# Performance work log

Measured on AMD Instinct MI355X. Metric: run time of the kernel, lower is better.

Reference implementation:

```python
import jax, jax.numpy as jnp
import numpy as np

ALPHA = 20.0 / 100.0  # dt / tau
ONE_MINUS_ALPHA = 1.0 - ALPHA
GAIN = 1.0


def setup_inputs() -> dict:
    key = jax.random.key(0)
    ks = jax.random.split(key, 6)
    seq_len, batch, input_size, hidden_size = 512, 64, 512, 1024
    s_in = 1.0 / np.sqrt(input_size)
    s_hh = 1.0 / np.sqrt(hidden_size)
    return {
        "x": jax.random.normal(ks[0], (seq_len, batch, input_size), jnp.float32),
        "hidden": jnp.zeros((batch, hidden_size), jnp.float32),
        "W_in": jax.random.normal(ks[1], (hidden_size, input_size), jnp.float32) * s_in,
        "b_in": jax.random.normal(ks[2], (hidden_size,), jnp.float32) * s_in,
        "W_hh": jax.random.normal(ks[3], (hidden_size, hidden_size), jnp.float32) * s_hh,
        "b_hh": jax.random.normal(ks[4], (hidden_size,), jnp.float32) * s_hh,
    }


def reference(x, hidden, W_in, b_in, W_hh, b_hh):
    # Precompute input projections for all timesteps in one big GEMM:
    # (T, B, I) @ (I, H) -> (T, B, H)
    x_proj = jnp.einsum("tbi,hi->tbh", x, W_in) + b_in

    def step(h, xp_t):
        pre = h @ W_hh.T + b_hh + xp_t  # (B, H)
        h_new = h * ONE_MINUS_ALPHA + ALPHA * jax.nn.sigmoid(GAIN * pre)
        return h_new, h_new

    h_last, output = jax.lax.scan(step, hidden, x_proj)
    return output, h_last
```

## Files before the change

kernel.cpp:

```cpp
#include <hip/hip_runtime.h>
#include <hip/hip_bf16.h>


typedef __attribute__((ext_vector_type(8))) short short8;
typedef __attribute__((ext_vector_type(4))) float f32x4;
typedef unsigned long long ull;

#define TT 512
#define BB 64
#define II 512
#define HH 1024

__device__ __forceinline__ short f2bf(float f) {
  unsigned u = __builtin_bit_cast(unsigned, f);
  u += 0x7fffu + ((u >> 16) & 1u);
  return (short)(u >> 16);
}

__device__ __forceinline__ short8 pack8(const float* p) {
  short8 s;
  s[0] = f2bf(p[0]); s[1] = f2bf(p[1]); s[2] = f2bf(p[2]); s[3] = f2bf(p[3]);
  s[4] = f2bf(p[4]); s[5] = f2bf(p[5]); s[6] = f2bf(p[6]); s[7] = f2bf(p[7]);
  return s;
}

__global__ __launch_bounds__(256, 1) void rnn_persist(
    const float* __restrict__ x, const float* __restrict__ h0,
    const float* __restrict__ Win, const float* __restrict__ bin,
    const float* __restrict__ Whh, const float* __restrict__ bhh,
    float* __restrict__ out, short* __restrict__ ring0,
    short* __restrict__ ring1, int* __restrict__ flags) {
  __shared__ short Wl[64 * 1024];
  __shared__ float Pr[4 * 16 * 68];

  const int bid = blockIdx.x;
  const int r = bid & 3, g = bid >> 2;
  const int tid = threadIdx.x;
  const int l = tid & 63, w = tid >> 6;
  const int lr = l & 15, lg = l >> 4;
  const int n0 = g * 64;

  for (int j = 0; j < 32; ++j) {
    int c = j * 256 + tid;
    int kc = c & 127, n = c >> 7;
    const float* src = Whh + (size_t)(n0 + n) * HH + kc * 8;
    float4 v0 = *(const float4*)src;
    float4 v1 = *(const float4*)(src + 4);
    short* d = Wl + (((size_t)kc * 64 + n) << 3);
    d[0] = f2bf(v0.x); d[1] = f2bf(v0.y); d[2] = f2bf(v0.z); d[3] = f2bf(v0.w);
    d[4] = f2bf(v1.x); d[5] = f2bf(v1.y); d[6] = f2bf(v1.z); d[7] = f2bf(v1.w);
  }

  short8 wf[4][4];
  #pragma unroll
  for (int nt = 0; nt < 4; ++nt) {
    #pragma unroll
    for (int kc = 0; kc < 4; ++kc) {
      const float* src = Win + (size_t)(n0 + nt * 16 + lr) * II + w * 128 + kc * 32 + lg * 8;
      float tmp[8];
      *(float4*)&tmp[0] = *(const float4*)src;
      *(float4*)&tmp[4] = *(const float4*)(src + 4);
      wf[nt][kc] = pack8(tmp);
    }
  }

  const int brow = tid >> 4;
  const int c0 = (tid & 15) * 4;
  const size_t oidx = (size_t)(16 * r + brow) * HH + n0 + c0;
  const size_t ringoff =
      (((size_t)(r * 128 + 8 * g + (c0 >> 3)) * 16 + brow) << 3) + (c0 & 7);

  f32x4 bias;
  #pragma unroll
  for (int k = 0; k < 4; ++k)
    bias[k] = bin[n0 + c0 + k] + bhh[n0 + c0 + k];

  f32x4 hpv;
  {
    float4 v = *(const float4*)(h0 + oidx);
    hpv[0] = v.x; hpv[1] = v.y; hpv[2] = v.z; hpv[3] = v.w;
    ull u = (ull)(unsigned short)f2bf(v.x)
          | ((ull)(unsigned short)f2bf(v.y) << 16)
          | ((ull)(unsigned short)f2bf(v.z) << 32)
          | ((ull)(unsigned short)f2bf(v.w) << 48);
    __hip_atomic_store((ull*)(ring0 + ringoff), u,
                       __ATOMIC_RELAXED, __HIP_MEMORY_SCOPE_AGENT);
  }

  float xs[4][8];
  {
    const float* xb = x + ((size_t)(16 * r + lr)) * II + w * 128 + lg * 8;
    #pragma unroll
    for (int kc = 0; kc < 4; ++kc) {
      *(float4*)&xs[kc][0] = *(const float4*)(xb + kc * 32);
      *(float4*)&xs[kc][4] = *(const float4*)(xb + kc * 32 + 4);
    }
  }

  __syncthreads();
  if (tid == 0)
    __hip_atomic_store(&flags[bid], 1, __ATOMIC_RELAXED, __HIP_MEMORY_SCOPE_AGENT);

  const int fidx = 16 * w + 4 * (l & 3) + r;
  const short* bW = Wl + ((((size_t)(32 * w + lg)) * 64 + lr) << 3);
  const size_t abase = ((((size_t)(r * 128 + 32 * w + lg)) * 16 + lr) << 3);

  for (int t = 0; t < TT; ++t) {
    short* rc = (t & 1) ? ring1 : ring0;
    short* rn = (t & 1) ? ring0 : ring1;
    float* outt = out + (size_t)t * (BB * HH);

    f32x4 acc[4];
    acc[0] = acc[1] = acc[2] = acc[3] = (f32x4){0.f, 0.f, 0.f, 0.f};
    #pragma unroll
    for (int kc = 0; kc < 4; ++kc) {
      short8 xa = pack8(xs[kc]);
      acc[0] = __builtin_amdgcn_mfma_f32_16x16x32_bf16(xa, wf[0][kc], acc[0], 0, 0, 0);
      acc[1] = __builtin_amdgcn_mfma_f32_16x16x32_bf16(xa, wf[1][kc], acc[1], 0, 0, 0);
      acc[2] = __builtin_amdgcn_mfma_f32_16x16x32_bf16(xa, wf[2][kc], acc[2], 0, 0, 0);
      acc[3] = __builtin_amdgcn_mfma_f32_16x16x32_bf16(xa, wf[3][kc], acc[3], 0, 0, 0);
    }

    {
      int target = t + 1;
      while (!__all(__hip_atomic_load(&flags[fidx], __ATOMIC_RELAXED,
                                      __HIP_MEMORY_SCOPE_AGENT) >= target))
        __builtin_amdgcn_s_sleep(1);
    }

    const short* ar = rc + abase;
    const short* ar2 = ar + 2048;
    int4 fa[8];
#define LDA(I, BASE, OFF) \
    asm volatile("global_load_dwordx4 %0, %1, off offset:%2 sc0 sc1" \
                 : "=v"(fa[I]) : "v"(BASE), "n"(OFF))
    LDA(0, ar, 0); LDA(1, ar, 1024); LDA(2, ar, 2048); LDA(3, ar, 3072);
    LDA(4, ar2, 0); LDA(5, ar2, 1024); LDA(6, ar2, 2048); LDA(7, ar2, 3072);
#undef LDA
    asm volatile("s_waitcnt vmcnt(0)" ::: "memory");
    __builtin_amdgcn_sched_barrier(0);

    #pragma unroll
    for (int i = 0; i < 8; ++i) {
      short8 a = __builtin_bit_cast(short8, fa[i]);
      acc[0] = __builtin_amdgcn_mfma_f32_16x16x32_bf16(
          a, *(const short8*)(bW + i * 2048 + 0),   acc[0], 0, 0, 0);
      acc[1] = __builtin_amdgcn_mfma_f32_16x16x32_bf16(
          a, *(const short8*)(bW + i * 2048 + 128), acc[1], 0, 0, 0);
      acc[2] = __builtin_amdgcn_mfma_f32_16x16x32_bf16(
          a, *(const short8*)(bW + i * 2048 + 256), acc[2], 0, 0, 0);
      acc[3] = __builtin_amdgcn_mfma_f32_16x16x32_bf16(
          a, *(const short8*)(bW + i * 2048 + 384), acc[3], 0, 0, 0);
    }

    float* pw = Pr + w * 1088;
    #pragma unroll
    for (int nt = 0; nt < 4; ++nt) {
      #pragma unroll
      for (int jj = 0; jj < 4; ++jj)
        pw[(lg * 4 + jj) * 68 + nt * 16 + lr] = acc[nt][jj];
    }
    __syncthreads();

    const float* pb = Pr + brow * 68 + c0;
    f32x4 s = *(const f32x4*)(pb)
            + *(const f32x4*)(pb + 1088)
            + *(const f32x4*)(pb + 2176)
            + *(const f32x4*)(pb + 3264);
    f32x4 hn;
    #pragma unroll
    for (int k = 0; k < 4; ++k) {
      float pre = s[k] + bias[k];
      float sg = 1.f / (1.f + __expf(-pre));
      hn[k] = 0.8f * hpv[k] + 0.2f * sg;
    }

    {
      ull u = (ull)(unsigned short)f2bf(hn[0])
            | ((ull)(unsigned short)f2bf(hn[1]) << 16)
            | ((ull)(unsigned short)f2bf(hn[2]) << 32)
            | ((ull)(unsigned short)f2bf(hn[3]) << 48);
      __hip_atomic_store((ull*)(rn + ringoff), u,
                         __ATOMIC_RELAXED, __HIP_MEMORY_SCOPE_AGENT);
    }
    asm volatile("s_waitcnt vmcnt(0)" ::: "memory");
    __syncthreads();
    if (tid == 0)
      __hip_atomic_store(&flags[bid], t + 2, __ATOMIC_RELAXED, __HIP_MEMORY_SCOPE_AGENT);

    *(float4*)(outt + oidx) = *(float4*)&hn;
    if (t == TT - 1) {
      *(float4*)(out + (size_t)TT * BB * HH + oidx) = *(float4*)&hn;
    } else {
      const float* xb = x + ((size_t)(t + 1) * BB + 16 * r + lr) * II + w * 128 + lg * 8;
      #pragma unroll
      for (int kc = 0; kc < 4; ++kc) {
        *(float4*)&xs[kc][0] = *(const float4*)(xb + kc * 32);
        *(float4*)&xs[kc][4] = *(const float4*)(xb + kc * 32 + 4);
      }
    }
    hpv = hn;
  }
}

extern "C" void kernel_launch(void* const* d_in, const int* in_sizes, int n_in,
                              void* d_out, int out_size, void* d_ws, size_t ws_size,
                              hipStream_t stream) {
  const float* x   = (const float*)d_in[0];
  const float* h0  = (const float*)d_in[1];
  const float* Win = (const float*)d_in[2];
  const float* bin = (const float*)d_in[3];
  const float* Whh = (const float*)d_in[4];
  const float* bhh = (const float*)d_in[5];
  float* out = (float*)d_out;

  int* flags = (int*)d_ws;
  short* ring0 = (short*)((char*)d_ws + 256);
  short* ring1 = ring0 + BB * HH;

  hipMemsetAsync(d_ws, 0, 256, stream);
  rnn_persist<<<dim3(64), 256, 0, stream>>>(x, h0, Win, bin, Whh, bhh,
                                            out, ring0, ring1, flags);
}
```

Before: 1.873 ms.

## Add producer warps computing input projection two steps ahead into shared ring

Doubles the block to 512 threads and splits it into 256 consumer threads, which run the recurrent matmul and update, and 256 producer threads. The producers compute the input projection x_t·W_in^T for step t+2 into a 3-slot shared-memory buffer. This takes the input-projection MFMAs and the x loads off the consumer's critical path between flag waits. In exchange there are more threads per CU and extra shared memory, and all 512 threads must reach the two __syncthreads per step, so the producers' work has to fit inside the consumers' step time.

```diff
diff --git a/kernel.cpp b/kernel.cpp
--- a/kernel.cpp
+++ b/kernel.cpp
@@ -24,7 +24,7 @@
   return s;
 }
 
-__global__ __launch_bounds__(256, 1) void rnn_persist(
+__global__ __launch_bounds__(512, 1) void rnn_persist(
     const float* __restrict__ x, const float* __restrict__ h0,
     const float* __restrict__ Win, const float* __restrict__ bin,
     const float* __restrict__ Whh, const float* __restrict__ bhh,
@@ -32,68 +32,82 @@
     short* __restrict__ ring1, int* __restrict__ flags) {
   __shared__ short Wl[64 * 1024];
   __shared__ float Pr[4 * 16 * 68];
+  __shared__ float Xp[3][16 * 68];
 
   const int bid = blockIdx.x;
   const int r = bid & 3, g = bid >> 2;
   const int tid = threadIdx.x;
-  const int l = tid & 63, w = tid >> 6;
+  const bool cons = (tid < 256);
+  const int l = tid & 63;
   const int lr = l & 15, lg = l >> 4;
   const int n0 = g * 64;
 
-  for (int j = 0; j < 32; ++j) {
-    int c = j * 256 + tid;
-    int kc = c & 127, n = c >> 7;
-    const float* src = Whh + (size_t)(n0 + n) * HH + kc * 8;
-    float4 v0 = *(const float4*)src;
-    float4 v1 = *(const float4*)(src + 4);
-    short* d = Wl + (((size_t)kc * 64 + n) << 3);
-    d[0] = f2bf(v0.x); d[1] = f2bf(v0.y); d[2] = f2bf(v0.z); d[3] = f2bf(v0.w);
-    d[4] = f2bf(v1.x); d[5] = f2bf(v1.y); d[6] = f2bf(v1.z); d[7] = f2bf(v1.w);
-  }
-
-  short8 wf[4][4];
-  #pragma unroll
-  for (int nt = 0; nt < 4; ++nt) {
+  f32x4 hpv, bias;
+  size_t oidx = 0, ringoff = 0;
+  int fidx = 0;
+  const short* bW = nullptr;
+  size_t abase = 0;
+  int brow = 0, c0 = 0;
+
+  short8 wf[16];
+  int pw = 0;
+
+  if (cons) {
+    const int w = tid >> 6;
+    for (int j = 0; j < 32; ++j) {
+      int c = j * 256 + tid;
+      int kc = c & 127, n = c >> 7;
+      const float* src = Whh + (size_t)(n0 + n) * HH + kc * 8;
+      float4 v0 = *(const float4*)src;
+      float4 v1 = *(const float4*)(src + 4);
+      short* d = Wl + (((size_t)kc * 64 + n) << 3);
+      d[0] = f2bf(v0.x); d[1] = f2bf(v0.y); d[2] = f2bf(v0.z); d[3] = f2bf(v0.w);
+      d[4] = f2bf(v1.x); d[5] = f2bf(v1.y); d[6] = f2bf(v1.z); d[7] = f2bf(v1.w);
+    }
+    brow = tid >> 4;
+    c0 = (tid & 15) * 4;
+    oidx = (size_t)(16 * r + brow) * HH + n0 + c0;
+    ringoff = (((size_t)(r * 128 + 8 * g + (c0 >> 3)) * 16 + brow) << 3) + (c0 & 7);
     #pragma unroll
-    for (int kc = 0; kc < 4; ++kc) {
-      const float* src = Win + (size_t)(n0 + nt * 16 + lr) * II + w * 128 + kc * 32 + lg * 8;
+    for (int k = 0; k < 4; ++k)
+      bias[k] = bin[n0 + c0 + k] + bhh[n0 + c0 + k];
+    {
+      float4 v = *(const float4*)(h0 + oidx);
+      hpv[0] = v.x; hpv[1] = v.y; hpv[2] = v.z; hpv[3] = v.w;
+      ull u = (ull)(unsigned short)f2bf(v.x)
+            | ((ull)(unsigned short)f2bf(v.y) << 16)
+            | ((ull)(unsigned short)f2bf(v.z) << 32)
+            | ((ull)(unsigned short)f2bf(v.w) << 48);
+      __hip_atomic_store((ull*)(ring0 + ringoff), u,
+                         __ATOMIC_RELAXED, __HIP_MEMORY_SCOPE_AGENT);
+    }
+    fidx = 16 * w + 4 * (l & 3) + r;
+    bW = Wl + ((((size_t)(32 * w + lg)) * 64 + lr) << 3);
+    abase = ((((size_t)(r * 128 + 32 * w + lg)) * 16 + lr) << 3);
+  } else {
+    pw = (tid >> 6) & 3;
+    #pragma unroll
+    for (int kidx = 0; kidx < 16; ++kidx) {
+      const float* src = Win + (size_t)(n0 + 16 * pw + lr) * II + kidx * 32 + lg * 8;
       float tmp[8];
       *(float4*)&tmp[0] = *(const float4*)src;
       *(float4*)&tmp[4] = *(const float4*)(src + 4);
-      wf[nt][kc] = pack8(tmp);
-    }
-  }
-
-  const int brow = tid >> 4;
-  const int c0 = (tid & 15) * 4;
-  const size_t oidx = (size_t)(16 * r + brow) * HH + n0 + c0;
-  const size_t ringoff =
-      (((size_t)(r * 128 + 8 * g + (c0 >> 3)) * 16 + brow) << 3) + (c0 & 7);
-
-  f32x4 bias;
-  #pragma unroll
-  for (int k = 0; k < 4; ++k)
-    bias[k] = bin[n0 + c0 + k] + bhh[n0 + c0 + k];
-
-  f32x4 hpv;
-  {
-    float4 v = *(const float4*)(h0 + oidx);
-    hpv[0] = v.x; hpv[1] = v.y; hpv[2] = v.z; hpv[3] = v.w;
-    ull u = (ull)(unsigned short)f2bf(v.x)
-          | ((ull)(unsigned short)f2bf(v.y) << 16)
-          | ((ull)(unsigned short)f2bf(v.z) << 32)
-          | ((ull)(unsigned short)f2bf(v.w) << 48);
-    __hip_atomic_store((ull*)(ring0 + ringoff), u,
-                       __ATOMIC_RELAXED, __HIP_MEMORY_SCOPE_AGENT);
-  }
-
-  float xs[4][8];
-  {
-    const float* xb = x + ((size_t)(16 * r + lr)) * II + w * 128 + lg * 8;
+      wf[kidx] = pack8(tmp);
+    }
     #pragma unroll
-    for (int kc = 0; kc < 4; ++kc) {
-      *(float4*)&xs[kc][0] = *(const float4*)(xb + kc * 32);
-      *(float4*)&xs[kc][4] = *(const float4*)(xb + kc * 32 + 4);
+    for (int t0 = 0; t0 < 2; ++t0) {
+      const float* xq = x + ((size_t)t0 * BB + 16 * r + lr) * II + lg * 8;
+      f32x4 pacc = (f32x4){0.f, 0.f, 0.f, 0.f};
+      #pragma unroll
+      for (int kidx = 0; kidx < 16; ++kidx) {
+        float tmp[8];
+        *(float4*)&tmp[0] = *(const float4*)(xq + kidx * 32);
+        *(float4*)&tmp[4] = *(const float4*)(xq + kidx * 32 + 4);
+        pacc = __builtin_amdgcn_mfma_f32_16x16x32_bf16(pack8(tmp), wf[kidx], pacc, 0, 0, 0);
+      }
+      #pragma unroll
+      for (int j = 0; j < 4; ++j)
+        Xp[t0][(lg * 4 + j) * 68 + 16 * pw + lr] = pacc[j];
     }
   }
 
@@ -101,105 +115,107 @@
   if (tid == 0)
     __hip_atomic_store(&flags[bid], 1, __ATOMIC_RELAXED, __HIP_MEMORY_SCOPE_AGENT);
 
-  const int fidx = 16 * w + 4 * (l & 3) + r;
-  const short* bW = Wl + ((((size_t)(32 * w + lg)) * 64 + lr) << 3);
-  const size_t abase = ((((size_t)(r * 128 + 32 * w + lg)) * 16 + lr) << 3);
-
   for (int t = 0; t < TT; ++t) {
-    short* rc = (t & 1) ? ring1 : ring0;
-    short* rn = (t & 1) ? ring0 : ring1;
-    float* outt = out + (size_t)t * (BB * HH);
-
     f32x4 acc[4];
-    acc[0] = acc[1] = acc[2] = acc[3] = (f32x4){0.f, 0.f, 0.f, 0.f};
-    #pragma unroll
-    for (int kc = 0; kc < 4; ++kc) {
-      short8 xa = pack8(xs[kc]);
-      acc[0] = __builtin_amdgcn_mfma_f32_16x16x32_bf16(xa, wf[0][kc], acc[0], 0, 0, 0);
-      acc[1] = __builtin_amdgcn_mfma_f32_16x16x32_bf16(xa, wf[1][kc], acc[1], 0, 0, 0);
-      acc[2] = __builtin_amdgcn_mfma_f32_16x16x32_bf16(xa, wf[2][kc], acc[2], 0, 0, 0);
-      acc[3] = __builtin_amdgcn_mfma_f32_16x16x32_bf16(xa, wf[3][kc], acc[3], 0, 0, 0);
-    }
-
-    {
-      int target = t + 1;
-      while (!__all(__hip_atomic_load(&flags[fidx], __ATOMIC_RELAXED,
-                                      __HIP_MEMORY_SCOPE_AGENT) >= target))
-        __builtin_amdgcn_s_sleep(1);
-    }
-
-    const short* ar = rc + abase;
-    const short* ar2 = ar + 2048;
-    int4 fa[8];
+    if (cons) {
+      short* rc = (t & 1) ? ring1 : ring0;
+      {
+        int target = t + 1;
+        while (!__all(__hip_atomic_load(&flags[fidx], __ATOMIC_RELAXED,
+                                        __HIP_MEMORY_SCOPE_AGENT) >= target))
+          __builtin_amdgcn_s_sleep(1);
+      }
+      const short* ar = rc + abase;
+      const short* ar2 = ar + 2048;
+      int4 fa[8];
 #define LDA(I, BASE, OFF) \
-    asm volatile("global_load_dwordx4 %0, %1, off offset:%2 sc0 sc1" \
-                 : "=v"(fa[I]) : "v"(BASE), "n"(OFF))
-    LDA(0, ar, 0); LDA(1, ar, 1024); LDA(2, ar, 2048); LDA(3, ar, 3072);
-    LDA(4, ar2, 0); LDA(5, ar2, 1024); LDA(6, ar2, 2048); LDA(7, ar2, 3072);
+      asm volatile("global_load_dwordx4 %0, %1, off offset:%2 sc0 sc1" \
+                   : "=v"(fa[I]) : "v"(BASE), "n"(OFF))
+      LDA(0, ar, 0); LDA(1, ar, 1024); LDA(2, ar, 2048); LDA(3, ar, 3072);
+      LDA(4, ar2, 0); LDA(5, ar2, 1024); LDA(6, ar2, 2048); LDA(7, ar2, 3072);
 #undef LDA
-    asm volatile("s_waitcnt vmcnt(0)" ::: "memory");
-    __builtin_amdgcn_sched_barrier(0);
-
-    #pragma unroll
-    for (int i = 0; i < 8; ++i) {
-      short8 a = __builtin_bit_cast(short8, fa[i]);
-      acc[0] = __builtin_amdgcn_mfma_f32_16x16x32_bf16(
-          a, *(const short8*)(bW + i * 2048 + 0),   acc[0], 0, 0, 0);
-      acc[1] = __builtin_amdgcn_mfma_f32_16x16x32_bf16(
-          a, *(const short8*)(bW + i * 2048 + 128), acc[1], 0, 0, 0);
-      acc[2] = __builtin_amdgcn_mfma_f32_16x16x32_bf16(
-          a, *(const short8*)(bW + i * 2048 + 256), acc[2], 0, 0, 0);
-      acc[3] = __builtin_amdgcn_mfma_f32_16x16x32_bf16(
-          a, *(const short8*)(bW + i * 2048 + 384), acc[3], 0, 0, 0);
-    }
-
-    float* pw = Pr + w * 1088;
-    #pragma unroll
-    for (int nt = 0; nt < 4; ++nt) {
-      #pragma unroll
-      for (int jj = 0; jj < 4; ++jj)
-        pw[(lg * 4 + jj) * 68 + nt * 16 + lr] = acc[nt][jj];
-    }
+      asm volatile("s_waitcnt vmcnt(0)" ::: "memory");
+      __builtin_amdgcn_sched_barrier(0);
+      acc[0] = acc[1] = acc[2] = acc[3] = (f32x4){0.f, 0.f, 0.f, 0.f};
+      #pragma unroll
+      for (int i = 0; i < 8; ++i) {
+        short8 a = __builtin_bit_cast(short8, fa[i]);
+        acc[0] = __builtin_amdgcn_mfma_f32_16x16x32_bf16(
+            a, *(const short8*)(bW + i * 2048 + 0),   acc[0], 0, 0, 0);
+        acc[1] = __builtin_amdgcn_mfma_f32_16x16x32_bf16(
+            a, *(const short8*)(bW + i * 2048 + 128), acc[1], 0, 0, 0);
+        acc[2] = __builtin_amdgcn_mfma_f32_16x16x32_bf16(
+            a, *(const short8*)(bW + i * 2048 + 256), acc[2], 0, 0, 0);
+        acc[3] = __builtin_amdgcn_mfma_f32_16x16x32_bf16(
+            a, *(const short8*)(bW + i * 2048 + 384), acc[3], 0, 0, 0);
+      }
+      {
+        const int w = tid >> 6;
+        float* pwr = Pr + w * 1088;
+        #pragma unroll
+        for (int nt = 0; nt < 4; ++nt) {
+          #pragma unroll
+          for (int jj = 0; jj < 4; ++jj)
+            pwr[(lg * 4 + jj) * 68 + nt * 16 + lr] = acc[nt][jj];
+        }
+      }
+    } else {
+      if (t + 2 < TT) {
+        const int wslot = (t + 2) % 3;
+        const float* xq = x + ((size_t)(t + 2) * BB + 16 * r + lr) * II + lg * 8;
+        f32x4 pacc = (f32x4){0.f, 0.f, 0.f, 0.f};
+        #pragma unroll
+        for (int kidx = 0; kidx < 16; ++kidx) {
+          float tmp[8];
+          *(float4*)&tmp[0] = *(const float4*)(xq + kidx * 32);
+          *(float4*)&tmp[4] = *(const float4*)(xq + kidx * 32 + 4);
+          pacc = __builtin_amdgcn_mfma_f32_16x16x32_bf16(pack8(tmp), wf[kidx], pacc, 0, 0, 0);
+        }
+        #pragma unroll
+        for (int j = 0; j < 4; ++j)
+          Xp[wslot][(lg * 4 + j) * 68 + 16 * pw + lr] = pacc[j];
+      }
+    }
+
     __syncthreads();
 
-    const float* pb = Pr + brow * 68 + c0;
-    f32x4 s = *(const f32x4*)(pb)
-            + *(const f32x4*)(pb + 1088)
-            + *(const f32x4*)(pb + 2176)
-            + *(const f32x4*)(pb + 3264);
     f32x4 hn;
-    #pragma unroll
-    for (int k = 0; k < 4; ++k) {
-      float pre = s[k] + bias[k];
-      float sg = 1.f / (1.f + __expf(-pre));
-      hn[k] = 0.8f * hpv[k] + 0.2f * sg;
-    }
-
-    {
+    if (cons) {
+      short* rn = (t & 1) ? ring0 : ring1;
+      const float* pb = Pr + brow * 68 + c0;
+      const float* xpb = &Xp[t % 3][brow * 68 + c0];
+      f32x4 s = *(const f32x4*)(pb)
+              + *(const f32x4*)(pb + 1088)
+              + *(const f32x4*)(pb + 2176)
+              + *(const f32x4*)(pb + 3264)
+              + *(const f32x4*)(xpb);
+      #pragma unroll
+      for (int k = 0; k < 4; ++k) {
+        float pre = s[k] + bias[k];
+        float sg = 1.f / (1.f + __expf(-pre));
+        hn[k] = 0.8f * hpv[k] + 0.2f * sg;
+      }
       ull u = (ull)(unsigned short)f2bf(hn[0])
             | ((ull)(unsigned short)f2bf(hn[1]) << 16)
             | ((ull)(unsigned short)f2bf(hn[2]) << 32)
             | ((ull)(unsigned short)f2bf(hn[3]) << 48);
       __hip_atomic_store((ull*)(rn + ringoff), u,
                          __ATOMIC_RELAXED, __HIP_MEMORY_SCOPE_AGENT);
-    }
-    asm volatile("s_waitcnt vmcnt(0)" ::: "memory");
+      asm volatile("s_waitcnt vmcnt(0)" ::: "memory");
+    }
+
     __syncthreads();
+
     if (tid == 0)
       __hip_atomic_store(&flags[bid], t + 2, __ATOMIC_RELAXED, __HIP_MEMORY_SCOPE_AGENT);
 
-    *(float4*)(outt + oidx) = *(float4*)&hn;
-    if (t == TT - 1) {
-      *(float4*)(out + (size_t)TT * BB * HH + oidx) = *(float4*)&hn;
-    } else {
-      const float* xb = x + ((size_t)(t + 1) * BB + 16 * r + lr) * II + w * 128 + lg * 8;
-      #pragma unroll
-      for (int kc = 0; kc < 4; ++kc) {
-        *(float4*)&xs[kc][0] = *(const float4*)(xb + kc * 32);
-        *(float4*)&xs[kc][4] = *(const float4*)(xb + kc * 32 + 4);
-      }
-    }
-    hpv = hn;
+    if (cons) {
+      float* outt = out + (size_t)t * (BB * HH);
+      *(float4*)(outt + oidx) = *(float4*)&hn;
+      if (t == TT - 1)
+        *(float4*)(out + (size_t)TT * BB * HH + oidx) = *(float4*)&hn;
+      hpv = hn;
+    }
   }
 }
 
@@ -219,6 +235,6 @@
   short* ring1 = ring0 + BB * HH;
 
   hipMemsetAsync(d_ws, 0, 256, stream);
-  rnn_persist<<<dim3(64), 256, 0, stream>>>(x, h0, Win, bin, Whh, bhh,
+  rnn_persist<<<dim3(64), 512, 0, stream>>>(x, h0, Win, bin, Whh, bhh,
                                             out, ring0, ring1, flags);
 }
```

Measured after the change: 2.802 ms. 49.6% more time.
